# Optimization experiments

Hardware: AMD Instinct MI355X
Metric: run time of the kernel (lower is better)

Reference implementation:

```python
import jax, jax.numpy as jnp
import numpy as np

N_USER, N_ITEM = 60000, 60000
N = N_USER + N_ITEM
E_BASE = 1500000
P = 200000
IN_DIM, HID, OUT = 128, 128, 64
K_MAX = 0.5


def setup_inputs() -> dict:
    key = jax.random.key(0)
    ks = jax.random.split(key, 20)
    feat_user = jax.random.normal(ks[0], (N_USER, 256), jnp.float32)
    feat_item = jax.random.normal(ks[1], (N_ITEM, 128), jnp.float32)
    src_b = jax.random.randint(ks[2], (E_BASE,), 0, N, jnp.int32)
    dst_b = jax.random.randint(ks[3], (E_BASE,), 0, N, jnp.int32)
    loops = jnp.arange(N, dtype=jnp.int32)  # dgl.add_self_loop
    src = jnp.concatenate([src_b, loops])
    dst = jnp.concatenate([dst_b, loops])
    pos_src = jax.random.randint(ks[4], (P,), 0, N, jnp.int32)
    pos_dst = jax.random.randint(ks[5], (P,), 0, N, jnp.int32)
    neg_src = jax.random.randint(ks[6], (P,), 0, N, jnp.int32)
    neg_dst = jax.random.randint(ks[7], (P,), 0, N, jnp.int32)
    s = 0.05
    W_user = jax.random.normal(ks[8], (256, IN_DIM), jnp.float32) * s
    b_user = jnp.zeros((IN_DIM,), jnp.float32)
    W_item = jax.random.normal(ks[9], (128, IN_DIM), jnp.float32) * s
    b_item = jnp.zeros((IN_DIM,), jnp.float32)
    W_gat = jax.random.normal(ks[10], (IN_DIM, HID), jnp.float32) * s
    attn_l = jax.random.normal(ks[11], (HID,), jnp.float32) * s
    attn_r = jax.random.normal(ks[12], (HID,), jnp.float32) * s
    gat_bias = jnp.zeros((HID,), jnp.float32)
    W_pred = jax.random.normal(ks[13], (HID, OUT), jnp.float32) * s
    b_pred = jnp.zeros((OUT,), jnp.float32)
    return {
        "feat_user": feat_user, "feat_item": feat_item,
        "W_user": W_user, "b_user": b_user, "W_item": W_item, "b_item": b_item,
        "W_gat": W_gat, "attn_l": attn_l, "attn_r": attn_r, "gat_bias": gat_bias,
        "W_pred": W_pred, "b_pred": b_pred,
        "src": src, "dst": dst,
        "pos_src": pos_src, "pos_dst": pos_dst,
        "neg_src": neg_src, "neg_dst": neg_dst,
        "alpha_T": 1,
    }


def _gat_conv(x, src, dst, W_gat, attn_l, attn_r, gat_bias):
    # DGL GATConv, 1 head: fc (no bias), additive attention, edge softmax over dst.
    z = x @ W_gat                              # [N, HID]
    el = z @ attn_l                            # [N]
    er = z @ attn_r                            # [N]
    e = jax.nn.leaky_relu(el[src] + er[dst], 0.2)   # [E]
    m = jax.ops.segment_max(e, dst, num_segments=N)  # per-dst max (self loops -> no empty segs)
    ex = jnp.exp(e - m[dst])
    ssum = jax.ops.segment_sum(ex, dst, num_segments=N)
    a = ex / ssum[dst]                          # edge softmax coeffs
    msg = z[src] * a[:, None]                   # [E, HID]
    out = jax.ops.segment_sum(msg, dst, num_segments=N) + gat_bias
    return jax.nn.elu(out)                      # activation=F.elu


def _hold_loss(score, k_T):
    l = jax.nn.log_sigmoid(score)
    hold = k_T * jnp.max(l)
    l = jnp.where(l > hold, 0.0, l)
    return -jnp.sum(l)


def reference(feat_user, feat_item, W_user, b_user, W_item, b_item,
              W_gat, attn_l, attn_r, gat_bias, W_pred, b_pred,
              src, dst, pos_src, pos_dst, neg_src, neg_dst, alpha_T):
    # per-type input projection then concat in ntype order (dgl.to_homogeneous)
    hu = feat_user @ W_user + b_user
    hi = feat_item @ W_item + b_item
    x = jnp.concatenate([hu, hi], axis=0)       # [N, IN_DIM]
    h = _gat_conv(x, src, dst, W_gat, attn_l, attn_r, gat_bias)
    pos_score = jnp.sum(h[pos_src] * h[pos_dst], axis=1)
    neg_score = jnp.sum(h[neg_src] * h[neg_dst], axis=1)
    k_T = K_MAX if K_MAX <= alpha_T else alpha_T   # k_T = min(k_max, alpha_T)
    loss = _hold_loss(pos_score, k_T) + _hold_loss(neg_score, k_T)
    out = h[:N_USER] @ W_pred + b_pred          # predict_type 'user' == type id 0
    return loss, out
```

## Files before the change

kernel.cpp:

```cpp
#include <hip/hip_runtime.h>
#include <hip/hip_bf16.h>
#include <math.h>

#define NUSER 60000
#define NITEM 60000
#define NNODE 120000
#define BSH 9
#define NB 235
#define PBSH 7
#define PB 938
#define CAP 8192

typedef __attribute__((ext_vector_type(8))) short bf16x8;
typedef __attribute__((ext_vector_type(4))) float f32x4;
typedef __attribute__((ext_vector_type(2))) float f32x2;
typedef __attribute__((ext_vector_type(4))) unsigned short u16x4;

__device__ __forceinline__ float leaky02(float x) { return x > 0.f ? x : 0.2f * x; }

__device__ __forceinline__ float inv_ord(unsigned int u) {
  unsigned int bits = (u & 0x80000000u) ? (u & 0x7FFFFFFFu) : ~u;
  return __uint_as_float(bits);
}
__device__ __forceinline__ unsigned int ord_of(float f) {
  unsigned int u = __float_as_uint(f);
  return (u & 0x80000000u) ? ~u : (u | 0x80000000u);
}
__device__ __forceinline__ short f2bs(float f) {
  __hip_bfloat16 h = __float2bfloat16(f);
  return *reinterpret_cast<short*>(&h);
}

__device__ __forceinline__ void f8fma(f32x2& acc, float w, unsigned int u) {
  f32x2 zz = __builtin_amdgcn_cvt_pk_f32_fp8(u, false);
  f32x2 ww; ww.x = w; ww.y = w;
  acc = __builtin_elementwise_fma(ww, zz, acc);
}
__device__ __forceinline__ void fp8dot(f32x2& acc, unsigned int ua, unsigned int ub) {
  f32x2 a0 = __builtin_amdgcn_cvt_pk_f32_fp8(ua, false);
  f32x2 a1 = __builtin_amdgcn_cvt_pk_f32_fp8(ua, true);
  f32x2 b0 = __builtin_amdgcn_cvt_pk_f32_fp8(ub, false);
  f32x2 b1 = __builtin_amdgcn_cvt_pk_f32_fp8(ub, true);
  acc = __builtin_elementwise_fma(a0, b0, acc);
  acc = __builtin_elementwise_fma(a1, b1, acc);
}

__global__ __launch_bounds__(256) void prep_count_kernel(
    const float* __restrict__ Wu, const float* __restrict__ bu, const float* __restrict__ Wi,
    const float* __restrict__ bi, const float* __restrict__ Wg, const float* __restrict__ Wp,
    __hip_bfloat16* __restrict__ Bp_u, __hip_bfloat16* __restrict__ Bp_i,
    __hip_bfloat16* __restrict__ Bp_p, float* __restrict__ bf_u, float* __restrict__ bf_i,
    const int* __restrict__ dst, int* __restrict__ btotal, int E,
    const int* __restrict__ ps, const int* __restrict__ ns, int* __restrict__ pbtotal, int P) {
  __shared__ int cnt[PB];
  if (blockIdx.x < 512) {
    int bid = blockIdx.x;
    for (int t = threadIdx.x; t < NB; t += 256) cnt[t] = 0;
    __syncthreads();
    for (int i = bid * 256 + threadIdx.x; i < E; i += 512 * 256)
      atomicAdd(&cnt[dst[i] >> BSH], 1);
    __syncthreads();
    for (int t = threadIdx.x; t < NB; t += 256)
      if (cnt[t]) atomicAdd(&btotal[t], cnt[t]);
    return;
  }
  if (blockIdx.x >= 737) {
    int bid = blockIdx.x - 737;
    int TOT = 2 * P;
    for (int t = threadIdx.x; t < PB; t += 256) cnt[t] = 0;
    __syncthreads();
    for (int i = bid * 256 + threadIdx.x; i < TOT; i += 128 * 256) {
      int a = (i < P) ? ps[i] : ns[i - P];
      atomicAdd(&cnt[a >> PBSH], 1);
    }
    __syncthreads();
    for (int t = threadIdx.x; t < PB; t += 256)
      if (cnt[t]) atomicAdd(&pbtotal[t], cnt[t]);
    return;
  }
  int t = (blockIdx.x - 512) * 256 + threadIdx.x;
  if (t < 32768) {
    int j = t & 7, lane = (t >> 3) & 63, rest = t >> 9;
    int nt = rest & 7, ks = rest >> 3;
    int k = ks * 32 + ((lane >> 4) << 3) + j;
    int n = nt * 16 + (lane & 15);
    float acc = 0.f;
#pragma unroll 8
    for (int jj = 0; jj < 128; ++jj) acc = fmaf(Wu[k * 128 + jj], Wg[jj * 128 + n], acc);
    Bp_u[t] = __float2bfloat16(acc);
  } else if (t < 49152) {
    int tt = t - 32768;
    int j = tt & 7, lane = (tt >> 3) & 63, rest = tt >> 9;
    int nt = rest & 7, ks = rest >> 3;
    int k = ks * 32 + ((lane >> 4) << 3) + j;
    int n = nt * 16 + (lane & 15);
    float acc = 0.f;
#pragma unroll 8
    for (int jj = 0; jj < 128; ++jj) acc = fmaf(Wi[k * 128 + jj], Wg[jj * 128 + n], acc);
    Bp_i[tt] = __float2bfloat16(acc);
  } else if (t < 57344) {
    int tt = t - 49152;
    int j = tt & 7, lane = (tt >> 3) & 63, rest = tt >> 9;
    int nt = rest & 3, ks = rest >> 2;
    int k = ks * 32 + ((lane >> 4) << 3) + j;
    int n = nt * 16 + (lane & 15);
    Bp_p[tt] = __float2bfloat16(Wp[k * 64 + n]);
  } else if (t < 57344 + 256) {
    int n = t - 57344;
    if (n < 128) {
      float acc = 0.f;
      for (int jj = 0; jj < 128; ++jj) acc = fmaf(bu[jj], Wg[jj * 128 + n], acc);
      bf_u[n] = acc;
    } else {
      int nn = n - 128;
      float acc = 0.f;
      for (int jj = 0; jj < 128; ++jj) acc = fmaf(bi[jj], Wg[jj * 128 + nn], acc);
      bf_i[nn] = acc;
    }
  }
}

__global__ void bscan_kernel(const int* __restrict__ btotal, int* __restrict__ bstart,
                             int* __restrict__ gcur, const int* __restrict__ pbtotal,
                             int* __restrict__ pbstart, int* __restrict__ pgcur) {
  __shared__ int s[256];
  int t = threadIdx.x;
  int v = (t < NB) ? btotal[t] : 0;
  s[t] = v;
  __syncthreads();
  for (int off = 1; off < 256; off <<= 1) {
    int a = (t >= off) ? s[t - off] : 0;
    __syncthreads();
    s[t] += a;
    __syncthreads();
  }
  int excl = s[t] - v;
  if (t < NB) { bstart[t] = excl; gcur[t] = excl; }
  if (t == NB - 1) bstart[NB] = s[t];
  __syncthreads();
  int v4[4], sum4 = 0;
#pragma unroll
  for (int k = 0; k < 4; ++k) {
    int idx = t * 4 + k;
    v4[k] = (idx < PB) ? pbtotal[idx] : 0;
    sum4 += v4[k];
  }
  s[t] = sum4;
  __syncthreads();
  for (int off = 1; off < 256; off <<= 1) {
    int a = (t >= off) ? s[t - off] : 0;
    __syncthreads();
    s[t] += a;
    __syncthreads();
  }
  int run = s[t] - sum4;
#pragma unroll
  for (int k = 0; k < 4; ++k) {
    int idx = t * 4 + k;
    if (idx < PB) { pbstart[idx] = run; pgcur[idx] = run; }
    run += v4[k];
  }
  if (t == 255) pbstart[PB] = s[255];
}

template <int K>
__device__ __forceinline__ void zgemm_body(
    char* smem, const float* __restrict__ A, const __hip_bfloat16* __restrict__ Bp,
    const float* __restrict__ bias, const float* __restrict__ al, const float* __restrict__ ar,
    unsigned char* __restrict__ z8, float* __restrict__ el, float* __restrict__ er, int M,
    int blk) {
  const int lane = threadIdx.x & 63, wv = threadIdx.x >> 6;
  const int t = threadIdx.x;
  int arow = blk * 64 + wv * 16 + (lane & 15);
  if (arow >= M) arow = M - 1;
  const float* a0 = A + (size_t)arow * K + ((lane >> 4) << 3);
  const bf16x8* bp = (const bf16x8*)Bp;
  f32x4 acc[8] = {};
#pragma unroll
  for (int ks = 0; ks < K / 32; ++ks) {
    float4 a1 = *(const float4*)(a0 + ks * 32);
    float4 a2 = *(const float4*)(a0 + ks * 32 + 4);
    bf16x8 af;
    af[0] = f2bs(a1.x); af[1] = f2bs(a1.y); af[2] = f2bs(a1.z); af[3] = f2bs(a1.w);
    af[4] = f2bs(a2.x); af[5] = f2bs(a2.y); af[6] = f2bs(a2.z); af[7] = f2bs(a2.w);
#pragma unroll
    for (int nt = 0; nt < 8; ++nt) {
      bf16x8 bfr = bp[(ks * 8 + nt) * 64 + lane];
      acc[nt] = __builtin_amdgcn_mfma_f32_16x16x32_bf16(af, bfr, acc[nt], 0, 0, 0);
    }
  }
  float(*lds2)[68] = (float(*)[68])smem;
  int row = t >> 2, qq = t & 3;
  int gm = blk * 64 + row;
  float pl = 0.f, pr = 0.f;
#pragma unroll
  for (int p = 0; p < 2; ++p) {
    __syncthreads();
#pragma unroll
    for (int nt = p * 4; nt < p * 4 + 4; ++nt) {
      float b = bias[nt * 16 + (lane & 15)];
#pragma unroll
      for (int r = 0; r < 4; ++r)
        lds2[wv * 16 + (lane >> 4) * 4 + r][(nt & 3) * 16 + (lane & 15)] = acc[nt][r] + b;
    }
    __syncthreads();
    if (gm < M) {
#pragma unroll
      for (int v4 = 0; v4 < 2; ++v4) {
        float f[8];
#pragma unroll
        for (int j = 0; j < 8; ++j) {
          f[j] = lds2[row][qq * 16 + v4 * 8 + j];
          int c = p * 64 + qq * 16 + v4 * 8 + j;
          pl = fmaf(f[j], al[c], pl);
          pr = fmaf(f[j], ar[c], pr);
        }
        unsigned int w0 = (unsigned int)__builtin_amdgcn_cvt_pk_fp8_f32(f[0], f[1], 0, false);
        w0 = (unsigned int)__builtin_amdgcn_cvt_pk_fp8_f32(f[2], f[3], (int)w0, true);
        unsigned int w1 = (unsigned int)__builtin_amdgcn_cvt_pk_fp8_f32(f[4], f[5], 0, false);
        w1 = (unsigned int)__builtin_amdgcn_cvt_pk_fp8_f32(f[6], f[7], (int)w1, true);
        uint2 st; st.x = w0; st.y = w1;
        *(uint2*)(z8 + (size_t)gm * 128 + p * 64 + qq * 16 + v4 * 8) = st;
      }
    }
  }
  pl += __shfl_xor(pl, 1, 64); pl += __shfl_xor(pl, 2, 64);
  pr += __shfl_xor(pr, 1, 64); pr += __shfl_xor(pr, 2, 64);
  if (qq == 0 && gm < M) { el[gm] = pl; er[gm] = pr; }
}

__global__ __launch_bounds__(256) void zgemm_scatter_kernel(
    const float* __restrict__ Au, const __hip_bfloat16* __restrict__ Bpu,
    const float* __restrict__ bfu, const float* __restrict__ Ai,
    const __hip_bfloat16* __restrict__ Bpi, const float* __restrict__ bfi,
    const float* __restrict__ al, const float* __restrict__ ar, unsigned char* __restrict__ z8,
    float* __restrict__ el, float* __restrict__ er, int SC, int PSC, int GU,
    const int* __restrict__ src, const int* __restrict__ dst, int* __restrict__ gcur,
    unsigned int* __restrict__ scratch, int E,
    const int* __restrict__ ps, const int* __restrict__ pd, const int* __restrict__ ns,
    const int* __restrict__ nd, int* __restrict__ pgcur, uint2* __restrict__ pairbuf, int P) {
  __shared__ __align__(16) char smem[17408];
  int bx = blockIdx.x;
  if (bx < SC) {
    int* cnt = (int*)smem;
    int* basep = cnt + NB;
    for (int t = threadIdx.x; t < NB; t += 256) cnt[t] = 0;
    __syncthreads();
    const int i0 = bx * 4096;
    unsigned int v_[16];
    int b_[16], r_[16];
#pragma unroll
    for (int j = 0; j < 16; ++j) {
      int i = i0 + j * 256 + threadIdx.x;
      b_[j] = -1;
      if (i < E) {
        int d = dst[i];
        int s = src[i];
        int b = d >> BSH;
        b_[j] = b;
        r_[j] = atomicAdd(&cnt[b], 1);
        v_[j] = (unsigned int)s | ((unsigned int)(d & 511) << 17);
      }
    }
    __syncthreads();
    for (int t = threadIdx.x; t < NB; t += 256)
      basep[t] = cnt[t] ? atomicAdd(&gcur[t], cnt[t]) : 0;
    __syncthreads();
#pragma unroll
    for (int j = 0; j < 16; ++j)
      if (b_[j] >= 0) scratch[basep[b_[j]] + r_[j]] = v_[j];
    return;
  }
  if (bx < SC + PSC) {
    int* cnt = (int*)smem;
    int* basep = cnt + PB;
    for (int t = threadIdx.x; t < PB; t += 256) cnt[t] = 0;
    __syncthreads();
    const int TOT = 2 * P;
    const int i0 = (bx - SC) * 4096;
    unsigned int x_[16], y_[16];
    int b_[16], r_[16];
#pragma unroll
    for (int j = 0; j < 16; ++j) {
      int i = i0 + j * 256 + threadIdx.x;
      b_[j] = -1;
      if (i < TOT) {
        int a, b, wh;
        if (i < P) { a = ps[i]; b = pd[i]; wh = 0; }
        else { a = ns[i - P]; b = nd[i - P]; wh = 1; }
        int bk = a >> PBSH;
        b_[j] = bk;
        r_[j] = atomicAdd(&cnt[bk], 1);
        x_[j] = (unsigned int)a | ((unsigned int)wh << 17);
        y_[j] = (unsigned int)b;
      }
    }
    __syncthreads();
    for (int t = threadIdx.x; t < PB; t += 256)
      basep[t] = cnt[t] ? atomicAdd(&pgcur[t], cnt[t]) : 0;
    __syncthreads();
#pragma unroll
    for (int j = 0; j < 16; ++j)
      if (b_[j] >= 0) pairbuf[basep[b_[j]] + r_[j]] = make_uint2(x_[j], y_[j]);
    return;
  }
  int gb = bx - SC - PSC;
  if (gb < GU)
    zgemm_body<256>(smem, Au, Bpu, bfu, al, ar, z8, el, er, NUSER, gb);
  else
    zgemm_body<128>(smem, Ai, Bpi, bfi, al, ar, z8 + (size_t)NUSER * 128, el + NUSER, er + NUSER,
                    NITEM, gb - GU);
}

__global__ __launch_bounds__(512) void bsort_kernel(const unsigned int* __restrict__ scratch,
                                                    const int* __restrict__ bstart,
                                                    int* __restrict__ offs, int* __restrict__ ssrc) {
  __shared__ unsigned int buf[CAP];
  __shared__ int cnt[512], scn[512], cur[512];
  int b = blockIdx.x, t = threadIdx.x;
  int s = bstart[b], e = bstart[b + 1], n = e - s;
  int d0 = b << BSH;
  int ndst = NNODE - d0;
  if (ndst > 512) ndst = 512;
  cnt[t] = 0;
  cur[t] = 0;
  __syncthreads();
  bool fit = (n <= CAP);
  if (fit) {
    for (int i = t; i < n; i += 512) {
      unsigned int v = scratch[s + i];
      buf[i] = v;
      atomicAdd(&cnt[v >> 17], 1);
    }
  } else {
    for (int i = t; i < n; i += 512) atomicAdd(&cnt[scratch[s + i] >> 17], 1);
  }
  __syncthreads();
  scn[t] = cnt[t];
  __syncthreads();
  for (int off = 1; off < 512; off <<= 1) {
    int a = (t >= off) ? scn[t - off] : 0;
    __syncthreads();
    scn[t] += a;
    __syncthreads();
  }
  int start = scn[t] - cnt[t];
  if (t < ndst) offs[d0 + t] = s + start;
  if (b == NB - 1 && t == 0) offs[NNODE] = e;
  __syncthreads();
  cnt[t] = start;
  __syncthreads();
  if (fit) {
    for (int i = t; i < n; i += 512) {
      unsigned int v = buf[i];
      int dl = v >> 17;
      int r = atomicAdd(&cur[dl], 1);
      ssrc[s + cnt[dl] + r] = (int)(v & 0x1FFFFu);
    }
  } else {
    for (int i = t; i < n; i += 512) {
      unsigned int v = scratch[s + i];
      int dl = v >> 17;
      int r = atomicAdd(&cur[dl], 1);
      ssrc[s + cnt[dl] + r] = (int)(v & 0x1FFFFu);
    }
  }
}

__global__ __launch_bounds__(256) void aggregate_kernel(
    const unsigned char* __restrict__ z8, const float* __restrict__ el,
    const float* __restrict__ er, const int* __restrict__ offs, const int* __restrict__ ssrc,
    const float* __restrict__ gat_bias, __hip_bfloat16* __restrict__ h,
    unsigned char* __restrict__ h8) {
  __shared__ __align__(16) float2 ew[4][128];
  int wv = threadIdx.x >> 6, lane = threadIdx.x & 63;
  int d = blockIdx.x * 4 + wv;
  int s0 = offs[d], s1 = offs[d + 1];
  int deg = s1 - s0;
  float erd = er[d];
  const unsigned short* zw = (const unsigned short*)z8;
  f32x2 acc = {0.f, 0.f};
  float ssum = 0.f;
  if (deg <= 128) {
    float w0 = 0.f, w1 = 0.f;
    int o0 = 0, o1 = 0;
    if (lane < deg) { int s = ssrc[s0 + lane]; o0 = s << 6; w0 = __expf(leaky02(el[s] + erd)); }
    if (64 + lane < deg) { int s = ssrc[s0 + 64 + lane]; o1 = s << 6; w1 = __expf(leaky02(el[s] + erd)); }
    ew[wv][lane] = make_float2(w0, __int_as_float(o0));
    ew[wv][64 + lane] = make_float2(w1, __int_as_float(o1));
    __builtin_amdgcn_wave_barrier();
    int i = 0;
    for (; i + 8 <= deg; i += 8) {
      float4 p0 = *(const float4*)&ew[wv][i];
      float4 p1 = *(const float4*)&ew[wv][i + 2];
      float4 p2 = *(const float4*)&ew[wv][i + 4];
      float4 p3 = *(const float4*)&ew[wv][i + 6];
      unsigned int u0 = zw[__float_as_uint(p0.y) + lane];
      unsigned int u1 = zw[__float_as_uint(p0.w) + lane];
      unsigned int u2 = zw[__float_as_uint(p1.y) + lane];
      unsigned int u3 = zw[__float_as_uint(p1.w) + lane];
      unsigned int u4 = zw[__float_as_uint(p2.y) + lane];
      unsigned int u5 = zw[__float_as_uint(p2.w) + lane];
      unsigned int u6 = zw[__float_as_uint(p3.y) + lane];
      unsigned int u7 = zw[__float_as_uint(p3.w) + lane];
      ssum += ((p0.x + p0.z) + (p1.x + p1.z)) + ((p2.x + p2.z) + (p3.x + p3.z));
      f8fma(acc, p0.x, u0); f8fma(acc, p0.z, u1);
      f8fma(acc, p1.x, u2); f8fma(acc, p1.z, u3);
      f8fma(acc, p2.x, u4); f8fma(acc, p2.z, u5);
      f8fma(acc, p3.x, u6); f8fma(acc, p3.z, u7);
    }
    for (; i + 2 <= deg; i += 2) {
      float4 p = *(const float4*)&ew[wv][i];
      unsigned int ua = zw[__float_as_uint(p.y) + lane];
      unsigned int ub = zw[__float_as_uint(p.w) + lane];
      ssum += p.x + p.z;
      f8fma(acc, p.x, ua); f8fma(acc, p.z, ub);
    }
    if (i < deg) {
      float2 pp = ew[wv][i];
      unsigned int u = zw[__float_as_uint(pp.y) + lane];
      ssum += pp.x;
      f8fma(acc, pp.x, u);
    }
  } else {
    for (int i2 = s0; i2 < s1; ++i2) {
      int s = ssrc[i2];
      float w = __expf(leaky02(el[s] + erd));
      ssum += w;
      unsigned int u = zw[((unsigned int)s << 6) + lane];
      f8fma(acc, w, u);
    }
  }
  float inv = 1.f / ssum;
  float o0f = acc.x * inv + gat_bias[lane * 2];
  float o1f = acc.y * inv + gat_bias[lane * 2 + 1];
  o0f = (o0f > 0.f) ? o0f : (__expf(o0f) - 1.f);
  o1f = (o1f > 0.f) ? o1f : (__expf(o1f) - 1.f);
  ushort2 ov;
  ov.x = (unsigned short)((unsigned int)f2bs(o0f) & 0xFFFFu);
  ov.y = (unsigned short)((unsigned int)f2bs(o1f) & 0xFFFFu);
  *(ushort2*)((unsigned short*)h + (size_t)d * 128 + lane * 2) = ov;
  int pk8 = __builtin_amdgcn_cvt_pk_fp8_f32(o0f, o1f, 0, false);
  *(unsigned short*)(h8 + (size_t)d * 128 + lane * 2) = (unsigned short)(pk8 & 0xFFFF);
}

__global__ __launch_bounds__(256) void scorepred_kernel(
    const unsigned char* __restrict__ h8, const uint2* __restrict__ pairbuf,
    const int* __restrict__ pbstart, float* __restrict__ l_all,
    unsigned int* __restrict__ maxacc,
    const __hip_bfloat16* __restrict__ h, const __hip_bfloat16* __restrict__ Bp,
    const float* __restrict__ bias, float* __restrict__ outp, int GP) {
  if ((int)blockIdx.x < GP) {
    const int lane = threadIdx.x & 63, wv = threadIdx.x >> 6;
    const int m0 = blockIdx.x * 64 + wv * 16;
    int arow = m0 + (lane & 15);
    if (arow >= NUSER) arow = NUSER - 1;
    const bf16x8* a0 = (const bf16x8*)(h + (size_t)arow * 128) + (lane >> 4);
    const bf16x8* bp = (const bf16x8*)Bp;
    f32x4 acc[4] = {};
#pragma unroll
    for (int ks = 0; ks < 4; ++ks) {
      bf16x8 af = a0[ks * 4];
#pragma unroll
      for (int nt = 0; nt < 4; ++nt) {
        bf16x8 bfr = bp[(ks * 4 + nt) * 64 + lane];
        acc[nt] = __builtin_amdgcn_mfma_f32_16x16x32_bf16(af, bfr, acc[nt], 0, 0, 0);
      }
    }
#pragma unroll
    for (int nt = 0; nt < 4; ++nt) {
      int col = nt * 16 + (lane & 15);
      float b = bias[col];
#pragma unroll
      for (int r = 0; r < 4; ++r) {
        int m = m0 + (lane >> 4) * 4 + r;
        if (m < NUSER) outp[(size_t)m * 64 + col] = acc[nt][r] + b;
      }
    }
    return;
  }
  const int sb = blockIdx.x - GP;
  const int g8 = threadIdx.x >> 3, l8 = threadIdx.x & 7;
  const uint4* h4 = (const uint4*)h8;
  const int sP = pbstart[sb], eP = pbstart[sb + 1];
  float mpos = -1e30f, mneg = -1e30f;

  int i = sP + g8;
  uint2 prC = make_uint2(0, 0);
  uint4 vaC = {0, 0, 0, 0}, vbC = {0, 0, 0, 0};
  if (i < eP) {
    prC = pairbuf[i];
    vaC = h4[(size_t)(prC.x & 0x1FFFFu) * 8 + l8];
    vbC = h4[(size_t)prC.y * 8 + l8];
  }
  int i1 = i + 32;
  uint2 prN = make_uint2(0, 0);
  if (i1 < eP) prN = pairbuf[i1];

  while (i < eP) {
    uint4 vaN = {0, 0, 0, 0}, vbN = {0, 0, 0, 0};
    if (i1 < eP) {
      vaN = h4[(size_t)(prN.x & 0x1FFFFu) * 8 + l8];
      vbN = h4[(size_t)prN.y * 8 + l8];
    }
    int i2 = i1 + 32;
    uint2 prN2 = make_uint2(0, 0);
    if (i2 < eP) prN2 = pairbuf[i2];
    f32x2 acc = {0.f, 0.f};
    fp8dot(acc, vaC.x, vbC.x);
    fp8dot(acc, vaC.y, vbC.y);
    fp8dot(acc, vaC.z, vbC.z);
    fp8dot(acc, vaC.w, vbC.w);
    float s = acc.x + acc.y;
    s += __shfl_xor(s, 1, 8);
    s += __shfl_xor(s, 2, 8);
    s += __shfl_xor(s, 4, 8);
    float lv = fminf(s, 0.f) - log1pf(__expf(-fabsf(s)));
    bool neg = (prC.x >> 17) & 1u;
    if (l8 == 0) l_all[i] = lv;
    if (neg) mneg = fmaxf(mneg, lv); else mpos = fmaxf(mpos, lv);
    i = i1; i1 = i2;
    prC = prN; prN = prN2;
    vaC = vaN; vbC = vbN;
  }
  __shared__ float red0[256], red1[256];
  red0[threadIdx.x] = mpos;
  red1[threadIdx.x] = mneg;
  __syncthreads();
  for (int off = 128; off; off >>= 1) {
    if (threadIdx.x < off) {
      red0[threadIdx.x] = fmaxf(red0[threadIdx.x], red0[threadIdx.x + off]);
      red1[threadIdx.x] = fmaxf(red1[threadIdx.x], red1[threadIdx.x + off]);
    }
    __syncthreads();
  }
  if (threadIdx.x == 0) {
    if (red0[0] > -1e29f) atomicMax(maxacc + 0, ord_of(red0[0]));
    if (red1[0] > -1e29f) atomicMax(maxacc + 1, ord_of(red1[0]));
  }
}

__global__ __launch_bounds__(256) void loss_sum_kernel(const float* __restrict__ l_all,
                                                       const uint2* __restrict__ pairbuf,
                                                       const unsigned int* __restrict__ maxacc,
                                                       const int* __restrict__ alpha,
                                                       float* __restrict__ sums,
                                                       unsigned int* __restrict__ fincnt,
                                                       float* __restrict__ out, int TOT) {
  __shared__ float sd0[256], sd1[256];
  float a = (float)alpha[0];
  float kT = (0.5f <= a) ? 0.5f : a;
  float hold0 = kT * inv_ord(maxacc[0]);
  float hold1 = kT * inv_ord(maxacc[1]);
  float s0 = 0.f, s1 = 0.f;
  for (int i = blockIdx.x * 256 + threadIdx.x; i < TOT; i += gridDim.x * 256) {
    float v = l_all[i];
    if ((pairbuf[i].x >> 17) & 1u) {
      if (!(v > hold1)) s1 += v;
    } else {
      if (!(v > hold0)) s0 += v;
    }
  }
  sd0[threadIdx.x] = s0;
  sd1[threadIdx.x] = s1;
  __syncthreads();
  for (int off = 128; off; off >>= 1) {
    if (threadIdx.x < off) {
      sd0[threadIdx.x] += sd0[threadIdx.x + off];
      sd1[threadIdx.x] += sd1[threadIdx.x + off];
    }
    __syncthreads();
  }
  if (threadIdx.x == 0) {
    atomicAdd(&sums[0], sd0[0]);
    atomicAdd(&sums[1], sd1[0]);
    __threadfence();
    unsigned int t = atomicAdd(fincnt, 1u);
    if (t == gridDim.x - 1) {
      float f0 = atomicAdd(&sums[0], 0.f);
      float f1 = atomicAdd(&sums[1], 0.f);
      out[0] = -(f0 + f1);
    }
  }
}

extern "C" void kernel_launch(void* const* d_in, const int* in_sizes, int n_in,
                              void* d_out, int out_size, void* d_ws, size_t ws_size,
                              hipStream_t stream) {
  const float* feat_user = (const float*)d_in[0];
  const float* feat_item = (const float*)d_in[1];
  const float* W_user = (const float*)d_in[2];
  const float* b_user = (const float*)d_in[3];
  const float* W_item = (const float*)d_in[4];
  const float* b_item = (const float*)d_in[5];
  const float* W_gat = (const float*)d_in[6];
  const float* attn_l = (const float*)d_in[7];
  const float* attn_r = (const float*)d_in[8];
  const float* gat_bias = (const float*)d_in[9];
  const float* W_pred = (const float*)d_in[10];
  const float* b_pred = (const float*)d_in[11];
  const int* src = (const int*)d_in[12];
  const int* dst = (const int*)d_in[13];
  const int* pos_src = (const int*)d_in[14];
  const int* pos_dst = (const int*)d_in[15];
  const int* neg_src = (const int*)d_in[16];
  const int* neg_dst = (const int*)d_in[17];
  const int* alpha = (const int*)d_in[18];
  const int E = in_sizes[12];
  const int P = in_sizes[14];
  const int TOT = 2 * P;

  char* p = (char*)d_ws;
  auto alloc = [&](size_t bytes) {
    char* r = p;
    p += (bytes + 255) & ~(size_t)255;
    return r;
  };
  unsigned char* z8 = (unsigned char*)alloc((size_t)NNODE * 128);
  __hip_bfloat16* h = (__hip_bfloat16*)alloc((size_t)NNODE * 128 * 2);
  unsigned char* h8 = (unsigned char*)alloc((size_t)NNODE * 128);
  float* el = (float*)alloc((size_t)NNODE * 4);
  float* er = (float*)alloc((size_t)NNODE * 4);
  __hip_bfloat16* Bp_u = (__hip_bfloat16*)alloc(256 * 128 * 2);
  __hip_bfloat16* Bp_i = (__hip_bfloat16*)alloc(128 * 128 * 2);
  __hip_bfloat16* Bp_p = (__hip_bfloat16*)alloc(128 * 64 * 2);
  float* bf_u = (float*)alloc(128 * 4);
  float* bf_i = (float*)alloc(128 * 4);
  int* offs = (int*)alloc((size_t)(NNODE + 4) * 4);
  int* ssrc = (int*)alloc((size_t)E * 4);
  unsigned int* scratch = (unsigned int*)alloc((size_t)E * 4);
  uint2* pairbuf = (uint2*)alloc((size_t)TOT * 8);
  float* l_all = (float*)alloc((size_t)TOT * 4);
  int* bstart = (int*)alloc((NB + 1) * 4);
  int* gcur = (int*)alloc(NB * 4);
  int* pbstart = (int*)alloc((PB + 1) * 4);
  int* pgcur = (int*)alloc(PB * 4);
  int* btotal = (int*)alloc((NB + PB + 8) * 4);
  int* pbtotal = btotal + NB;
  unsigned int* maxacc = (unsigned int*)(pbtotal + PB);
  float* sums = (float*)(maxacc + 2);
  unsigned int* fincnt = (unsigned int*)(sums + 2);

  hipMemsetAsync(btotal, 0, (NB + PB + 8) * 4, stream);

  prep_count_kernel<<<512 + 225 + 128, 256, 0, stream>>>(
      W_user, b_user, W_item, b_item, W_gat, W_pred, Bp_u, Bp_i, Bp_p, bf_u, bf_i, dst, btotal, E,
      pos_src, neg_src, pbtotal, P);
  bscan_kernel<<<1, 256, 0, stream>>>(btotal, bstart, gcur, pbtotal, pbstart, pgcur);
  const int GU = (NUSER + 63) / 64, GI = (NITEM + 63) / 64;
  const int SC = (E + 4095) / 4096;
  const int PSC = (TOT + 4095) / 4096;
  zgemm_scatter_kernel<<<SC + PSC + GU + GI, 256, 0, stream>>>(
      feat_user, Bp_u, bf_u, feat_item, Bp_i, bf_i, attn_l, attn_r, z8, el, er, SC, PSC, GU, src,
      dst, gcur, scratch, E, pos_src, pos_dst, neg_src, neg_dst, pgcur, pairbuf, P);
  bsort_kernel<<<NB, 512, 0, stream>>>(scratch, bstart, offs, ssrc);
  aggregate_kernel<<<NNODE / 4, 256, 0, stream>>>(z8, el, er, offs, ssrc, gat_bias, h, h8);
  const int GP = (NUSER + 63) / 64;
  scorepred_kernel<<<GP + PB, 256, 0, stream>>>(h8, pairbuf, pbstart, l_all, maxacc, h, Bp_p,
                                                b_pred, (float*)d_out + 1, GP);
  loss_sum_kernel<<<1024, 256, 0, stream>>>(l_all, pairbuf, maxacc, alpha, sums, fincnt,
                                            (float*)d_out, TOT);

  (void)n_in; (void)out_size; (void)ws_size;
}
```

Measured before the change: 233.3 us.

## Split scatter out of zgemm kernel and prefetch A chunks in GEMM loop

Separates the edge/pair bucket-scatter blocks from the projection GEMM into their own kernel, so the GEMM kernel no longer carries the scatter's branches, registers and shared-memory layout. The GEMM inner loop now loads all A values for a 128-wide K chunk up front and prefetches the next chunk while the MFMAs run on the current one. In exchange, the two workloads no longer run concurrently within one launch, there is an extra launch, and the prefetch buffers raise register pressure.

```diff
diff --git a/kernel.cpp b/kernel.cpp
--- a/kernel.cpp
+++ b/kernel.cpp
@@ -163,6 +163,75 @@
   if (t == 255) pbstart[PB] = s[255];
 }
 
+__global__ __launch_bounds__(256) void scatter_kernel(
+    const int* __restrict__ src, const int* __restrict__ dst, int* __restrict__ gcur,
+    unsigned int* __restrict__ scratch, int E, int SC,
+    const int* __restrict__ ps, const int* __restrict__ pd, const int* __restrict__ ns,
+    const int* __restrict__ nd, int* __restrict__ pgcur, uint2* __restrict__ pairbuf, int P) {
+  __shared__ int smem2[2 * PB];
+  int bx = blockIdx.x;
+  if (bx < SC) {
+    int* cnt = smem2;
+    int* basep = smem2 + NB;
+    for (int t = threadIdx.x; t < NB; t += 256) cnt[t] = 0;
+    __syncthreads();
+    const int i0 = bx * 4096;
+    unsigned int v_[16];
+    int b_[16], r_[16];
+#pragma unroll
+    for (int j = 0; j < 16; ++j) {
+      int i = i0 + j * 256 + threadIdx.x;
+      b_[j] = -1;
+      if (i < E) {
+        int d = dst[i];
+        int s = src[i];
+        int b = d >> BSH;
+        b_[j] = b;
+        r_[j] = atomicAdd(&cnt[b], 1);
+        v_[j] = (unsigned int)s | ((unsigned int)(d & 511) << 17);
+      }
+    }
+    __syncthreads();
+    for (int t = threadIdx.x; t < NB; t += 256)
+      basep[t] = cnt[t] ? atomicAdd(&gcur[t], cnt[t]) : 0;
+    __syncthreads();
+#pragma unroll
+    for (int j = 0; j < 16; ++j)
+      if (b_[j] >= 0) scratch[basep[b_[j]] + r_[j]] = v_[j];
+    return;
+  }
+  int* cnt = smem2;
+  int* basep = smem2 + PB;
+  for (int t = threadIdx.x; t < PB; t += 256) cnt[t] = 0;
+  __syncthreads();
+  const int TOT = 2 * P;
+  const int i0 = (bx - SC) * 4096;
+  unsigned int x_[16], y_[16];
+  int b_[16], r_[16];
+#pragma unroll
+  for (int j = 0; j < 16; ++j) {
+    int i = i0 + j * 256 + threadIdx.x;
+    b_[j] = -1;
+    if (i < TOT) {
+      int a, b, wh;
+      if (i < P) { a = ps[i]; b = pd[i]; wh = 0; }
+      else { a = ns[i - P]; b = nd[i - P]; wh = 1; }
+      int bk = a >> PBSH;
+      b_[j] = bk;
+      r_[j] = atomicAdd(&cnt[bk], 1);
+      x_[j] = (unsigned int)a | ((unsigned int)wh << 17);
+      y_[j] = (unsigned int)b;
+    }
+  }
+  __syncthreads();
+  for (int t = threadIdx.x; t < PB; t += 256)
+    basep[t] = cnt[t] ? atomicAdd(&pgcur[t], cnt[t]) : 0;
+  __syncthreads();
+#pragma unroll
+  for (int j = 0; j < 16; ++j)
+    if (b_[j] >= 0) pairbuf[basep[b_[j]] + r_[j]] = make_uint2(x_[j], y_[j]);
+}
+
 template <int K>
 __device__ __forceinline__ void zgemm_body(
     char* smem, const float* __restrict__ A, const __hip_bfloat16* __restrict__ Bp,
@@ -173,20 +242,38 @@
   const int t = threadIdx.x;
   int arow = blk * 64 + wv * 16 + (lane & 15);
   if (arow >= M) arow = M - 1;
-  const float* a0 = A + (size_t)arow * K + ((lane >> 4) << 3);
+  const float* a0p = A + (size_t)arow * K + ((lane >> 4) << 3);
   const bf16x8* bp = (const bf16x8*)Bp;
   f32x4 acc[8] = {};
-#pragma unroll
-  for (int ks = 0; ks < K / 32; ++ks) {
-    float4 a1 = *(const float4*)(a0 + ks * 32);
-    float4 a2 = *(const float4*)(a0 + ks * 32 + 4);
-    bf16x8 af;
-    af[0] = f2bs(a1.x); af[1] = f2bs(a1.y); af[2] = f2bs(a1.z); af[3] = f2bs(a1.w);
-    af[4] = f2bs(a2.x); af[5] = f2bs(a2.y); af[6] = f2bs(a2.z); af[7] = f2bs(a2.w);
-#pragma unroll
-    for (int nt = 0; nt < 8; ++nt) {
-      bf16x8 bfr = bp[(ks * 8 + nt) * 64 + lane];
-      acc[nt] = __builtin_amdgcn_mfma_f32_16x16x32_bf16(af, bfr, acc[nt], 0, 0, 0);
+  constexpr int NCH = K / 128;
+  float4 ab[8];
+#pragma unroll
+  for (int q = 0; q < 8; ++q)
+    ab[q] = *(const float4*)(a0p + (q >> 1) * 32 + (q & 1) * 4);
+#pragma unroll
+  for (int c = 0; c < NCH; ++c) {
+    float4 an[8];
+    if (c + 1 < NCH) {
+#pragma unroll
+      for (int q = 0; q < 8; ++q)
+        an[q] = *(const float4*)(a0p + (c + 1) * 128 + (q >> 1) * 32 + (q & 1) * 4);
+    }
+#pragma unroll
+    for (int s = 0; s < 4; ++s) {
+      int ks = c * 4 + s;
+      float4 a1 = ab[s * 2], a2 = ab[s * 2 + 1];
+      bf16x8 af;
+      af[0] = f2bs(a1.x); af[1] = f2bs(a1.y); af[2] = f2bs(a1.z); af[3] = f2bs(a1.w);
+      af[4] = f2bs(a2.x); af[5] = f2bs(a2.y); af[6] = f2bs(a2.z); af[7] = f2bs(a2.w);
+#pragma unroll
+      for (int nt = 0; nt < 8; ++nt) {
+        bf16x8 bfr = bp[(ks * 8 + nt) * 64 + lane];
+        acc[nt] = __builtin_amdgcn_mfma_f32_16x16x32_bf16(af, bfr, acc[nt], 0, 0, 0);
+      }
+    }
+    if (c + 1 < NCH) {
+#pragma unroll
+      for (int q = 0; q < 8; ++q) ab[q] = an[q];
     }
   }
   float(*lds2)[68] = (float(*)[68])smem;
@@ -229,82 +316,14 @@
   if (qq == 0 && gm < M) { el[gm] = pl; er[gm] = pr; }
 }
 
-__global__ __launch_bounds__(256) void zgemm_scatter_kernel(
+__global__ __launch_bounds__(256) void zgemm_kernel(
     const float* __restrict__ Au, const __hip_bfloat16* __restrict__ Bpu,
     const float* __restrict__ bfu, const float* __restrict__ Ai,
     const __hip_bfloat16* __restrict__ Bpi, const float* __restrict__ bfi,
     const float* __restrict__ al, const float* __restrict__ ar, unsigned char* __restrict__ z8,
-    float* __restrict__ el, float* __restrict__ er, int SC, int PSC, int GU,
-    const int* __restrict__ src, const int* __restrict__ dst, int* __restrict__ gcur,
-    unsigned int* __restrict__ scratch, int E,
-    const int* __restrict__ ps, const int* __restrict__ pd, const int* __restrict__ ns,
-    const int* __restrict__ nd, int* __restrict__ pgcur, uint2* __restrict__ pairbuf, int P) {
+    float* __restrict__ el, float* __restrict__ er, int GU) {
   __shared__ __align__(16) char smem[17408];
-  int bx = blockIdx.x;
-  if (bx < SC) {
-    int* cnt = (int*)smem;
-    int* basep = cnt + NB;
-    for (int t = threadIdx.x; t < NB; t += 256) cnt[t] = 0;
-    __syncthreads();
-    const int i0 = bx * 4096;
-    unsigned int v_[16];
-    int b_[16], r_[16];
-#pragma unroll
-    for (int j = 0; j < 16; ++j) {
-      int i = i0 + j * 256 + threadIdx.x;
-      b_[j] = -1;
-      if (i < E) {
-        int d = dst[i];
-        int s = src[i];
-        int b = d >> BSH;
-        b_[j] = b;
-        r_[j] = atomicAdd(&cnt[b], 1);
-        v_[j] = (unsigned int)s | ((unsigned int)(d & 511) << 17);
-      }
-    }
-    __syncthreads();
-    for (int t = threadIdx.x; t < NB; t += 256)
-      basep[t] = cnt[t] ? atomicAdd(&gcur[t], cnt[t]) : 0;
-    __syncthreads();
-#pragma unroll
-    for (int j = 0; j < 16; ++j)
-      if (b_[j] >= 0) scratch[basep[b_[j]] + r_[j]] = v_[j];
-    return;
-  }
-  if (bx < SC + PSC) {
-    int* cnt = (int*)smem;
-    int* basep = cnt + PB;
-    for (int t = threadIdx.x; t < PB; t += 256) cnt[t] = 0;
-    __syncthreads();
-    const int TOT = 2 * P;
-    const int i0 = (bx - SC) * 4096;
-    unsigned int x_[16], y_[16];
-    int b_[16], r_[16];
-#pragma unroll
-    for (int j = 0; j < 16; ++j) {
-      int i = i0 + j * 256 + threadIdx.x;
-      b_[j] = -1;
-      if (i < TOT) {
-        int a, b, wh;
-        if (i < P) { a = ps[i]; b = pd[i]; wh = 0; }
-        else { a = ns[i - P]; b = nd[i - P]; wh = 1; }
-        int bk = a >> PBSH;
-        b_[j] = bk;
-        r_[j] = atomicAdd(&cnt[bk], 1);
-        x_[j] = (unsigned int)a | ((unsigned int)wh << 17);
-        y_[j] = (unsigned int)b;
-      }
-    }
-    __syncthreads();
-    for (int t = threadIdx.x; t < PB; t += 256)
-      basep[t] = cnt[t] ? atomicAdd(&pgcur[t], cnt[t]) : 0;
-    __syncthreads();
-#pragma unroll
-    for (int j = 0; j < 16; ++j)
-      if (b_[j] >= 0) pairbuf[basep[b_[j]] + r_[j]] = make_uint2(x_[j], y_[j]);
-    return;
-  }
-  int gb = bx - SC - PSC;
+  int gb = blockIdx.x;
   if (gb < GU)
     zgemm_body<256>(smem, Au, Bpu, bfu, al, ar, z8, el, er, NUSER, gb);
   else
@@ -647,12 +666,13 @@
       W_user, b_user, W_item, b_item, W_gat, W_pred, Bp_u, Bp_i, Bp_p, bf_u, bf_i, dst, btotal, E,
       pos_src, neg_src, pbtotal, P);
   bscan_kernel<<<1, 256, 0, stream>>>(btotal, bstart, gcur, pbtotal, pbstart, pgcur);
-  const int GU = (NUSER + 63) / 64, GI = (NITEM + 63) / 64;
   const int SC = (E + 4095) / 4096;
   const int PSC = (TOT + 4095) / 4096;
-  zgemm_scatter_kernel<<<SC + PSC + GU + GI, 256, 0, stream>>>(
-      feat_user, Bp_u, bf_u, feat_item, Bp_i, bf_i, attn_l, attn_r, z8, el, er, SC, PSC, GU, src,
-      dst, gcur, scratch, E, pos_src, pos_dst, neg_src, neg_dst, pgcur, pairbuf, P);
+  scatter_kernel<<<SC + PSC, 256, 0, stream>>>(src, dst, gcur, scratch, E, SC, pos_src, pos_dst,
+                                               neg_src, neg_dst, pgcur, pairbuf, P);
+  const int GU = (NUSER + 63) / 64, GI = (NITEM + 63) / 64;
+  zgemm_kernel<<<GU + GI, 256, 0, stream>>>(feat_user, Bp_u, bf_u, feat_item, Bp_i, bf_i, attn_l,
+                                            attn_r, z8, el, er, GU);
   bsort_kernel<<<NB, 512, 0, stream>>>(scratch, bstart, offs, ssrc);
   aggregate_kernel<<<NNODE / 4, 256, 0, stream>>>(z8, el, er, offs, ssrc, gat_bias, h, h8);
   const int GP = (NUSER + 63) / 64;
```

Measured after the change: 244.3 us. 4.7% more time.
